# Kernel optimization log

Measured on AMD Instinct MI355X. Metric: run time of the kernel, lower is better.

Reference implementation:

```python
import jax, jax.numpy as jnp
import numpy as np

N_NODES = 50000
N_EDGES = 250000
N_GRAPHS = 512
F_IN = 32
F_EDGE = 16
LATENT = 32
EMBED = 128


def setup_inputs() -> dict:
    key = jax.random.key(0)
    ks = jax.random.split(key, 10)
    x = jax.random.normal(ks[0], (N_NODES, F_IN), dtype=jnp.float32)
    edge_index = jax.random.randint(ks[1], (2, N_EDGES), 0, N_NODES, dtype=jnp.int64)
    edge_attr = jax.random.normal(ks[2], (N_EDGES, F_EDGE), dtype=jnp.float32)
    batch = jnp.sort(jax.random.randint(ks[3], (N_NODES,), 0, N_GRAPHS, dtype=jnp.int64))
    s = 0.05
    W1 = jax.random.normal(ks[4], (F_EDGE, LATENT), dtype=jnp.float32) * s
    b1 = jnp.zeros((LATENT,), jnp.float32)
    W2 = jax.random.normal(ks[5], (LATENT, F_IN * LATENT), dtype=jnp.float32) * s
    b2 = jnp.zeros((F_IN * LATENT,), jnp.float32)
    root = jax.random.normal(ks[6], (F_IN, LATENT), dtype=jnp.float32) * s
    conv_bias = jnp.zeros((LATENT,), jnp.float32)
    fc_w = jax.random.normal(ks[7], (LATENT, EMBED), dtype=jnp.float32) * s
    fc_b = jnp.zeros((EMBED,), jnp.float32)
    return dict(x=x, edge_index=edge_index, edge_attr=edge_attr, batch=batch,
                W1=W1, b1=b1, W2=W2, b2=b2, root=root, conv_bias=conv_bias,
                fc_w=fc_w, fc_b=fc_b)


def reference(x, edge_index, edge_attr, batch, W1, b1, W2, b2, root, conv_bias, fc_w, fc_b):
    src, dst = edge_index[0], edge_index[1]
    # edge MLP: [E, F_edge] -> [E, F_in*latent] -> [E, F_in, latent]
    h = jax.nn.relu(edge_attr @ W1 + b1)
    ew = (h @ W2 + b2).reshape(-1, F_IN, LATENT)
    # per-edge matvec: message_e = x[src_e] @ W_e
    msg = jnp.einsum('ef,efl->el', x[src], ew)
    # scatter-add to target nodes (NNConv default aggr='add')
    agg = jax.ops.segment_sum(msg, dst, num_segments=N_NODES)
    node = jax.nn.relu(agg + x @ root + conv_bias)
    # global mean pool per graph
    sums = jax.ops.segment_sum(node, batch, num_segments=N_GRAPHS)
    cnts = jax.ops.segment_sum(jnp.ones((node.shape[0],), node.dtype), batch, num_segments=N_GRAPHS)
    pooled = sums / jnp.maximum(cnts, 1.0)[:, None]
    return jax.nn.relu(pooled) @ fc_w + fc_b
```

## Files before the change

### kernel.cpp

```cpp
#include <hip/hip_runtime.h>

#define N_NODES 50000
#define N_EDGES 250000
#define N_GRAPHS 512
#define F_IN 32
#define F_EDGE 16
#define LATENT 32
#define EMBED 128
#define E_BLK 128
#define N_EBLK ((N_EDGES + E_BLK - 1) / E_BLK)
#define KW 1056
#define HS_STRIDE 36

typedef unsigned short ushort;
typedef unsigned int uint;
typedef _Float16 half8v __attribute__((ext_vector_type(8)));
typedef _Float16 half2v __attribute__((ext_vector_type(2)));
typedef __attribute__((ext_vector_type(4))) float f32x4;

union UH8 { half8v h8; half2v h2[4]; ushort u[8]; uint q[4]; };
union UH2 { half2v h2; uint q; };

__device__ inline ushort f2h_bits(float f) {
    _Float16 h = (_Float16)f;
    return *reinterpret_cast<ushort*>(&h);
}

__global__ void prep_kernel(const float* __restrict__ x, const float* __restrict__ W2,
                            const float* __restrict__ b2, ushort* __restrict__ xh,
                            ushort* __restrict__ W2T, float4* __restrict__ agg4,
                            float* __restrict__ pool, float* __restrict__ pcnt) {
    int i = blockIdx.x * blockDim.x + threadIdx.x;
    if (i < (N_NODES * F_IN) / 4) {
        float4 v = ((const float4*)x)[i];
        union { ushort u[4]; uint2 q; } pk;
        pk.u[0] = f2h_bits(v.x); pk.u[1] = f2h_bits(v.y);
        pk.u[2] = f2h_bits(v.z); pk.u[3] = f2h_bits(v.w);
        ((uint2*)xh)[i] = pk.q;
    }
    if (i < (N_NODES * LATENT) / 4) agg4[i] = make_float4(0.f, 0.f, 0.f, 0.f);
    if (i < 32 * 1024) {
        int kk = i >> 5, l = i & 31;
        W2T[l * KW + kk] = f2h_bits(W2[i]);
    }
    if (i < 1024) {
        int f = i >> 5, l = i & 31;
        W2T[l * KW + 1024 + f] = f2h_bits(b2[i]);
    }
    if (i < N_GRAPHS * LATENT) pool[i] = 0.f;
    if (i < N_GRAPHS) pcnt[i] = 0.f;
}

__global__ __launch_bounds__(256) void edge_mfma_kernel(
    const ushort* __restrict__ xh, const int* __restrict__ ei,
    const float* __restrict__ ea, const float* __restrict__ W1,
    const float* __restrict__ b1, const ushort* __restrict__ W2T,
    float* __restrict__ agg)
{
    __shared__ __attribute__((aligned(16))) uint Hs2[E_BLK * HS_STRIDE];
    __shared__ __attribute__((aligned(16))) ushort W2q[32 * 256];

    const int t = threadIdx.x;
    const int e0 = blockIdx.x * E_BLK;
    const int wv = t >> 6, lane = t & 63;
    const int g = lane >> 4, j16 = lane & 15;

    UH8 bw[2];
    #pragma unroll
    for (int nt = 0; nt < 2; ++nt) {
        #pragma unroll
        for (int b = 0; b < 8; ++b) {
            float w = (g < 2) ? W1[(8 * g + b) * LATENT + nt * 16 + j16] : 0.f;
            bw[nt].u[b] = f2h_bits(w);
        }
    }
    float b1v[2] = { b1[j16], b1[16 + j16] };

    #pragma unroll
    for (int mt = 0; mt < 2; ++mt) {
        int mtg = 2 * wv + mt;
        int rowA = mtg * 16 + j16;
        int e = e0 + rowA; if (e >= N_EDGES) e = N_EDGES - 1;
        UH8 ae;
        if (g < 2) {
            const float4* p = (const float4*)(ea + (size_t)e * F_EDGE + 8 * g);
            float4 va = p[0], vb = p[1];
            ae.u[0] = f2h_bits(va.x); ae.u[1] = f2h_bits(va.y);
            ae.u[2] = f2h_bits(va.z); ae.u[3] = f2h_bits(va.w);
            ae.u[4] = f2h_bits(vb.x); ae.u[5] = f2h_bits(vb.y);
            ae.u[6] = f2h_bits(vb.z); ae.u[7] = f2h_bits(vb.w);
        } else {
            ae.q[0] = 0; ae.q[1] = 0; ae.q[2] = 0; ae.q[3] = 0;
        }
        #pragma unroll
        for (int nt = 0; nt < 2; ++nt) {
            f32x4 hacc = (f32x4){0.f, 0.f, 0.f, 0.f};
            hacc = __builtin_amdgcn_mfma_f32_16x16x32_f16(ae.h8, bw[nt].h8, hacc, 0, 0, 0);
            #pragma unroll
            for (int v = 0; v < 4; ++v) {
                int rowD = mtg * 16 + 4 * g + v;
                int col = nt * 16 + j16;
                float hval = fmaxf(hacc[v] + b1v[nt], 0.f);
                uint hb = (uint)f2h_bits(hval);
                Hs2[rowD * HS_STRIDE + col] = hb * 0x10001u;
            }
        }
    }
    if (t < E_BLK) Hs2[t * HS_STRIDE + 32] = 0x3C003C00u;

    f32x4 acc[2][2];
    #pragma unroll
    for (int a = 0; a < 2; ++a)
        #pragma unroll
        for (int b = 0; b < 2; ++b) acc[a][b] = (f32x4){0.f, 0.f, 0.f, 0.f};

    UH8 xf[2];
    int myrow[2];
    #pragma unroll
    for (int mt = 0; mt < 2; ++mt) {
        int row = (2 * wv + mt) * 16 + j16;
        myrow[mt] = row;
        int e = e0 + row; if (e >= N_EDGES) e = N_EDGES - 1;
        int src = ei[e];
        uint4 raw = *(const uint4*)(xh + (size_t)src * F_IN + 8 * g);
        xf[mt].q[0] = raw.x; xf[mt].q[1] = raw.y; xf[mt].q[2] = raw.z; xf[mt].q[3] = raw.w;
    }

    {
        UH8 bx0, bx1;
        *(uint4*)bx0.q = *(const uint4*)(W2T + (size_t)j16 * KW + 1024 + 8 * g);
        *(uint4*)bx1.q = *(const uint4*)(W2T + (size_t)(16 + j16) * KW + 1024 + 8 * g);
        #pragma unroll
        for (int mt = 0; mt < 2; ++mt) {
            acc[mt][0] = __builtin_amdgcn_mfma_f32_16x16x32_f16(xf[mt].h8, bx0.h8, acc[mt][0], 0, 0, 0);
            acc[mt][1] = __builtin_amdgcn_mfma_f32_16x16x32_f16(xf[mt].h8, bx1.h8, acc[mt][1], 0, 0, 0);
        }
    }

    __syncthreads();

    for (int q = 0; q < 4; ++q) {
        if (q) __syncthreads();
        #pragma unroll
        for (int c = 0; c < 4; ++c) {
            int ch = c * 256 + t;
            int lbyte = ch * 16;
            int jrow = lbyte >> 9;
            int off = lbyte & 511;
            uint4 val = *(const uint4*)((const char*)W2T + (size_t)jrow * (KW * 2) + q * 512 + off);
            *(uint4*)((char*)W2q + jrow * 512 + (off ^ ((jrow & 7) << 4))) = val;
        }
        __syncthreads();

        uint hb[2][8];
        #pragma unroll
        for (int mt = 0; mt < 2; ++mt) {
            const uint* hp = Hs2 + myrow[mt] * HS_STRIDE + q * 8;
            uint4 a = *(const uint4*)hp;
            uint4 b = *(const uint4*)(hp + 4);
            hb[mt][0] = a.x; hb[mt][1] = a.y; hb[mt][2] = a.z; hb[mt][3] = a.w;
            hb[mt][4] = b.x; hb[mt][5] = b.y; hb[mt][6] = b.z; hb[mt][7] = b.w;
        }

        #pragma unroll
        for (int kst = 0; kst < 8; ++kst) {
            int kb = kst * 64 + g * 16;
            UH8 bf0, bf1;
            *(uint4*)bf0.q = *(const uint4*)((const char*)W2q + j16 * 512 + (kb ^ ((j16 & 7) << 4)));
            *(uint4*)bf1.q = *(const uint4*)((const char*)W2q + (16 + j16) * 512 + (kb ^ ((j16 & 7) << 4)));
            #pragma unroll
            for (int mt = 0; mt < 2; ++mt) {
                UH2 h2; h2.q = hb[mt][kst];
                UH8 af;
                #pragma unroll
                for (int p = 0; p < 4; ++p) af.h2[p] = h2.h2 * xf[mt].h2[p];
                acc[mt][0] = __builtin_amdgcn_mfma_f32_16x16x32_f16(af.h8, bf0.h8, acc[mt][0], 0, 0, 0);
                acc[mt][1] = __builtin_amdgcn_mfma_f32_16x16x32_f16(af.h8, bf1.h8, acc[mt][1], 0, 0, 0);
            }
        }
    }

    #pragma unroll
    for (int mt = 0; mt < 2; ++mt) {
        int rowb = (2 * wv + mt) * 16 + 4 * g;
        #pragma unroll
        for (int v = 0; v < 4; ++v) {
            int e = e0 + rowb + v;
            if (e < N_EDGES) {
                int dst = ei[N_EDGES + e];
                atomicAdd(&agg[(size_t)dst * LATENT + j16],      acc[mt][0][v]);
                atomicAdd(&agg[(size_t)dst * LATENT + 16 + j16], acc[mt][1][v]);
            }
        }
    }
}

#define VN 8
__global__ __launch_bounds__(256) void nodepool_kernel(
    const float* __restrict__ x, const float* __restrict__ agg,
    const float* __restrict__ root, const float* __restrict__ cbias,
    const int* __restrict__ batch, float* __restrict__ pool,
    float* __restrict__ pcnt)
{
    int t = threadIdx.x;
    int l = t & 31;
    int stripe = t >> 5;
    int v0 = (blockIdx.x * 8 + stripe) * VN;
    float rc[F_IN];
    #pragma unroll
    for (int f = 0; f < F_IN; ++f) rc[f] = root[f * LATENT + l];
    float cbl = cbias[l];

    float sum = 0.f, cnt = 0.f;
    int gcur = -1;
    for (int i = 0; i < VN; ++i) {
        int v = v0 + i;
        if (v >= N_NODES) break;
        int g = batch[v];
        if (g != gcur) {
            if (gcur >= 0) {
                atomicAdd(&pool[gcur * LATENT + l], sum);
                if (l == 0) atomicAdd(&pcnt[gcur], cnt);
            }
            gcur = g; sum = 0.f; cnt = 0.f;
        }
        float xv = x[(size_t)v * F_IN + l];
        float a = agg[(size_t)v * LATENT + l] + cbl;
        #pragma unroll
        for (int f = 0; f < F_IN; ++f) {
            float xfv = __shfl(xv, (t & 32) | f);
            a += xfv * rc[f];
        }
        sum += fmaxf(a, 0.f);
        cnt += 1.f;
    }
    if (gcur >= 0) {
        atomicAdd(&pool[gcur * LATENT + l], sum);
        if (l == 0) atomicAdd(&pcnt[gcur], cnt);
    }
}

__global__ void final_kernel(const float* __restrict__ pool, const float* __restrict__ pcnt,
                             const float* __restrict__ fcw, const float* __restrict__ fcb,
                             float* __restrict__ out)
{
    int t = blockIdx.x * blockDim.x + threadIdx.x;
    int gr = t >> 7, j = t & 127;
    if (gr >= N_GRAPHS) return;
    float inv = 1.0f / fmaxf(pcnt[gr], 1.0f);
    float o = fcb[j];
    #pragma unroll 8
    for (int l = 0; l < LATENT; ++l) {
        float pv = fmaxf(pool[gr * LATENT + l] * inv, 0.0f);
        o += pv * fcw[l * EMBED + j];
    }
    out[gr * EMBED + j] = o;
}

extern "C" void kernel_launch(void* const* d_in, const int* in_sizes, int n_in,
                              void* d_out, int out_size, void* d_ws, size_t ws_size,
                              hipStream_t stream)
{
    const float* x     = (const float*)d_in[0];
    const int*   ei    = (const int*)d_in[1];
    const float* ea    = (const float*)d_in[2];
    const int*   batch = (const int*)d_in[3];
    const float* W1    = (const float*)d_in[4];
    const float* b1    = (const float*)d_in[5];
    const float* W2    = (const float*)d_in[6];
    const float* b2    = (const float*)d_in[7];
    const float* root  = (const float*)d_in[8];
    const float* cb    = (const float*)d_in[9];
    const float* fcw   = (const float*)d_in[10];
    const float* fcb   = (const float*)d_in[11];
    float* out = (float*)d_out;

    char* w = (char*)d_ws;
    auto alloc = [&](size_t bytes) {
        char* p = w;
        w += (bytes + 255) & ~size_t(255);
        return p;
    };
    ushort* W2T  = (ushort*)alloc((size_t)32 * KW * 2);
    ushort* xh   = (ushort*)alloc((size_t)N_NODES * F_IN * 2);
    float*  agg  = (float*)alloc((size_t)N_NODES * LATENT * 4);
    float*  pool = (float*)alloc(N_GRAPHS * LATENT * 4);
    float*  pcnt = (float*)alloc(N_GRAPHS * 4);

    prep_kernel<<<1563, 256, 0, stream>>>(x, W2, b2, xh, W2T, (float4*)agg, pool, pcnt);
    edge_mfma_kernel<<<N_EBLK, 256, 0, stream>>>(xh, ei, ea, W1, b1, W2T, agg);
    nodepool_kernel<<<(N_NODES + 8 * VN - 1) / (8 * VN), 256, 0, stream>>>(
        x, agg, root, cb, batch, pool, pcnt);
    final_kernel<<<(N_GRAPHS * EMBED + 255) / 256, 256, 0, stream>>>(pool, pcnt, fcw, fcb, out);
}
```

Measured before the change: 77.57 us.

## Bucket edges by destination tile and fuse node update with edge kernel

Builds a CSR-like bucketing of edges by destination-node tile (64 nodes) with histogram, scan and scatter kernels. The edge kernel then processes each tile's edges, accumulates messages in shared-memory atomics, and performs the root transform, ReLU and pooling in the same block. This removes the global agg buffer, its zeroing and the global float atomics. In exchange it adds three small kernels (one single-block scan), indirect gathers through csr, partially filled 128-edge chunks, and uneven per-tile work.

New measurement: 249.0 us. 221% more time.

```diff
diff --git a/kernel.cpp b/kernel.cpp
--- a/kernel.cpp
+++ b/kernel.cpp
@@ -7,10 +7,12 @@
 #define F_EDGE 16
 #define LATENT 32
 #define EMBED 128
-#define E_BLK 128
-#define N_EBLK ((N_EDGES + E_BLK - 1) / E_BLK)
+#define DT 64
+#define NB ((N_NODES + DT - 1) / DT)
+#define EC 128
 #define KW 1056
 #define HS_STRIDE 36
+#define AGG_S 33
 
 typedef unsigned short ushort;
 typedef unsigned int uint;
@@ -28,7 +30,7 @@
 
 __global__ void prep_kernel(const float* __restrict__ x, const float* __restrict__ W2,
                             const float* __restrict__ b2, ushort* __restrict__ xh,
-                            ushort* __restrict__ W2T, float4* __restrict__ agg4,
+                            ushort* __restrict__ W2T, int* __restrict__ deg,
                             float* __restrict__ pool, float* __restrict__ pcnt) {
     int i = blockIdx.x * blockDim.x + threadIdx.x;
     if (i < (N_NODES * F_IN) / 4) {
@@ -38,7 +40,6 @@
         pk.u[2] = f2h_bits(v.z); pk.u[3] = f2h_bits(v.w);
         ((uint2*)xh)[i] = pk.q;
     }
-    if (i < (N_NODES * LATENT) / 4) agg4[i] = make_float4(0.f, 0.f, 0.f, 0.f);
     if (i < 32 * 1024) {
         int kk = i >> 5, l = i & 31;
         W2T[l * KW + kk] = f2h_bits(W2[i]);
@@ -47,23 +48,77 @@
         int f = i >> 5, l = i & 31;
         W2T[l * KW + 1024 + f] = f2h_bits(b2[i]);
     }
+    if (i < NB) deg[i] = 0;
     if (i < N_GRAPHS * LATENT) pool[i] = 0.f;
     if (i < N_GRAPHS) pcnt[i] = 0.f;
+}
+
+__global__ void hist_kernel(const int* __restrict__ ei, int* __restrict__ deg) {
+    int e = blockIdx.x * blockDim.x + threadIdx.x;
+    if (e < N_EDGES) atomicAdd(&deg[ei[N_EDGES + e] / DT], 1);
+}
+
+__global__ __launch_bounds__(1024) void scan_kernel(const int* __restrict__ deg,
+                                                    int* __restrict__ off,
+                                                    int* __restrict__ cursor) {
+    __shared__ int wsum[16];
+    int t = threadIdx.x;
+    int d = (t < NB) ? deg[t] : 0;
+    int lane = t & 63, wid = t >> 6;
+    int inc = d;
+    #pragma unroll
+    for (int s = 1; s < 64; s <<= 1) {
+        int o = __shfl_up(inc, s);
+        if (lane >= s) inc += o;
+    }
+    if (lane == 63) wsum[wid] = inc;
+    __syncthreads();
+    if (t < 16) {
+        int w = wsum[t];
+        int winc = w;
+        #pragma unroll
+        for (int s = 1; s < 16; s <<= 1) {
+            int o = __shfl_up(winc, s);
+            if (t >= s) winc += o;
+        }
+        wsum[t] = winc - w;
+    }
+    __syncthreads();
+    int base = wsum[wid] + (inc - d);
+    if (t < NB) { off[t] = base; cursor[t] = base; }
+    if (t == 1023) off[NB] = base + d;
+}
+
+__global__ void scatter_kernel(const int* __restrict__ ei, int* __restrict__ cursor,
+                               int* __restrict__ csr) {
+    int e = blockIdx.x * blockDim.x + threadIdx.x;
+    if (e < N_EDGES) {
+        int p = atomicAdd(&cursor[ei[N_EDGES + e] / DT], 1);
+        csr[p] = e;
+    }
 }
 
 __global__ __launch_bounds__(256) void edge_mfma_kernel(
     const ushort* __restrict__ xh, const int* __restrict__ ei,
     const float* __restrict__ ea, const float* __restrict__ W1,
     const float* __restrict__ b1, const ushort* __restrict__ W2T,
-    float* __restrict__ agg)
+    const int* __restrict__ off, const int* __restrict__ csr,
+    const float* __restrict__ x, const float* __restrict__ root,
+    const float* __restrict__ cbias, const int* __restrict__ batch,
+    float* __restrict__ pool, float* __restrict__ pcnt)
 {
-    __shared__ __attribute__((aligned(16))) uint Hs2[E_BLK * HS_STRIDE];
+    __shared__ __attribute__((aligned(16))) uint Hs2[EC * HS_STRIDE];
     __shared__ __attribute__((aligned(16))) ushort W2q[32 * 256];
+    __shared__ float aggL[DT * AGG_S];
 
     const int t = threadIdx.x;
-    const int e0 = blockIdx.x * E_BLK;
+    const int v0 = blockIdx.x * DT;
     const int wv = t >> 6, lane = t & 63;
     const int g = lane >> 4, j16 = lane & 15;
+    const int estart = off[blockIdx.x];
+    const int eend = off[blockIdx.x + 1];
+
+    for (int i = t; i < DT * AGG_S; i += 256) aggL[i] = 0.f;
 
     UH8 bw[2];
     #pragma unroll
@@ -75,168 +130,168 @@
         }
     }
     float b1v[2] = { b1[j16], b1[16 + j16] };
-
-    #pragma unroll
-    for (int mt = 0; mt < 2; ++mt) {
-        int mtg = 2 * wv + mt;
-        int rowA = mtg * 16 + j16;
-        int e = e0 + rowA; if (e >= N_EDGES) e = N_EDGES - 1;
-        UH8 ae;
-        if (g < 2) {
-            const float4* p = (const float4*)(ea + (size_t)e * F_EDGE + 8 * g);
-            float4 va = p[0], vb = p[1];
-            ae.u[0] = f2h_bits(va.x); ae.u[1] = f2h_bits(va.y);
-            ae.u[2] = f2h_bits(va.z); ae.u[3] = f2h_bits(va.w);
-            ae.u[4] = f2h_bits(vb.x); ae.u[5] = f2h_bits(vb.y);
-            ae.u[6] = f2h_bits(vb.z); ae.u[7] = f2h_bits(vb.w);
-        } else {
-            ae.q[0] = 0; ae.q[1] = 0; ae.q[2] = 0; ae.q[3] = 0;
-        }
-        #pragma unroll
-        for (int nt = 0; nt < 2; ++nt) {
-            f32x4 hacc = (f32x4){0.f, 0.f, 0.f, 0.f};
-            hacc = __builtin_amdgcn_mfma_f32_16x16x32_f16(ae.h8, bw[nt].h8, hacc, 0, 0, 0);
-            #pragma unroll
-            for (int v = 0; v < 4; ++v) {
-                int rowD = mtg * 16 + 4 * g + v;
-                int col = nt * 16 + j16;
-                float hval = fmaxf(hacc[v] + b1v[nt], 0.f);
-                uint hb = (uint)f2h_bits(hval);
-                Hs2[rowD * HS_STRIDE + col] = hb * 0x10001u;
-            }
-        }
-    }
-    if (t < E_BLK) Hs2[t * HS_STRIDE + 32] = 0x3C003C00u;
-
-    f32x4 acc[2][2];
-    #pragma unroll
-    for (int a = 0; a < 2; ++a)
-        #pragma unroll
-        for (int b = 0; b < 2; ++b) acc[a][b] = (f32x4){0.f, 0.f, 0.f, 0.f};
-
-    UH8 xf[2];
-    int myrow[2];
-    #pragma unroll
-    for (int mt = 0; mt < 2; ++mt) {
-        int row = (2 * wv + mt) * 16 + j16;
-        myrow[mt] = row;
-        int e = e0 + row; if (e >= N_EDGES) e = N_EDGES - 1;
-        int src = ei[e];
-        uint4 raw = *(const uint4*)(xh + (size_t)src * F_IN + 8 * g);
-        xf[mt].q[0] = raw.x; xf[mt].q[1] = raw.y; xf[mt].q[2] = raw.z; xf[mt].q[3] = raw.w;
-    }
-
-    {
-        UH8 bx0, bx1;
-        *(uint4*)bx0.q = *(const uint4*)(W2T + (size_t)j16 * KW + 1024 + 8 * g);
-        *(uint4*)bx1.q = *(const uint4*)(W2T + (size_t)(16 + j16) * KW + 1024 + 8 * g);
+    UH8 bx0, bx1;
+    *(uint4*)bx0.q = *(const uint4*)(W2T + (size_t)j16 * KW + 1024 + 8 * g);
+    *(uint4*)bx1.q = *(const uint4*)(W2T + (size_t)(16 + j16) * KW + 1024 + 8 * g);
+
+    __syncthreads();
+
+    for (int cs = estart; cs < eend; cs += EC) {
+        int nE = eend - cs; if (nE > EC) nE = EC;
+
+        #pragma unroll
+        for (int mt = 0; mt < 2; ++mt) {
+            int mtg = 2 * wv + mt;
+            int rowA = mtg * 16 + j16;
+            int p = cs + rowA; if (p >= eend) p = eend - 1;
+            int e = csr[p];
+            UH8 ae;
+            if (g < 2) {
+                const float4* pp = (const float4*)(ea + (size_t)e * F_EDGE + 8 * g);
+                float4 va = pp[0], vb = pp[1];
+                ae.u[0] = f2h_bits(va.x); ae.u[1] = f2h_bits(va.y);
+                ae.u[2] = f2h_bits(va.z); ae.u[3] = f2h_bits(va.w);
+                ae.u[4] = f2h_bits(vb.x); ae.u[5] = f2h_bits(vb.y);
+                ae.u[6] = f2h_bits(vb.z); ae.u[7] = f2h_bits(vb.w);
+            } else {
+                ae.q[0] = 0; ae.q[1] = 0; ae.q[2] = 0; ae.q[3] = 0;
+            }
+            #pragma unroll
+            for (int nt = 0; nt < 2; ++nt) {
+                f32x4 hacc = (f32x4){0.f, 0.f, 0.f, 0.f};
+                hacc = __builtin_amdgcn_mfma_f32_16x16x32_f16(ae.h8, bw[nt].h8, hacc, 0, 0, 0);
+                #pragma unroll
+                for (int v = 0; v < 4; ++v) {
+                    int rowD = mtg * 16 + 4 * g + v;
+                    int col = nt * 16 + j16;
+                    float hval = fmaxf(hacc[v] + b1v[nt], 0.f);
+                    uint hb = (uint)f2h_bits(hval);
+                    Hs2[rowD * HS_STRIDE + col] = hb * 0x10001u;
+                }
+            }
+        }
+        if (t < EC) Hs2[t * HS_STRIDE + 32] = 0x3C003C00u;
+
+        f32x4 acc[2][2];
+        #pragma unroll
+        for (int a = 0; a < 2; ++a)
+            #pragma unroll
+            for (int b = 0; b < 2; ++b) acc[a][b] = (f32x4){0.f, 0.f, 0.f, 0.f};
+
+        UH8 xf[2];
+        int myrow[2];
+        #pragma unroll
+        for (int mt = 0; mt < 2; ++mt) {
+            int row = (2 * wv + mt) * 16 + j16;
+            myrow[mt] = row;
+            int p = cs + row; if (p >= eend) p = eend - 1;
+            int src = ei[csr[p]];
+            uint4 raw = *(const uint4*)(xh + (size_t)src * F_IN + 8 * g);
+            xf[mt].q[0] = raw.x; xf[mt].q[1] = raw.y; xf[mt].q[2] = raw.z; xf[mt].q[3] = raw.w;
+        }
+
         #pragma unroll
         for (int mt = 0; mt < 2; ++mt) {
             acc[mt][0] = __builtin_amdgcn_mfma_f32_16x16x32_f16(xf[mt].h8, bx0.h8, acc[mt][0], 0, 0, 0);
             acc[mt][1] = __builtin_amdgcn_mfma_f32_16x16x32_f16(xf[mt].h8, bx1.h8, acc[mt][1], 0, 0, 0);
         }
-    }
-
-    __syncthreads();
-
-    for (int q = 0; q < 4; ++q) {
-        if (q) __syncthreads();
-        #pragma unroll
-        for (int c = 0; c < 4; ++c) {
-            int ch = c * 256 + t;
-            int lbyte = ch * 16;
-            int jrow = lbyte >> 9;
-            int off = lbyte & 511;
-            uint4 val = *(const uint4*)((const char*)W2T + (size_t)jrow * (KW * 2) + q * 512 + off);
-            *(uint4*)((char*)W2q + jrow * 512 + (off ^ ((jrow & 7) << 4))) = val;
-        }
+
         __syncthreads();
 
-        uint hb[2][8];
+        for (int q = 0; q < 4; ++q) {
+            if (q) __syncthreads();
+            #pragma unroll
+            for (int c = 0; c < 4; ++c) {
+                int ch = c * 256 + t;
+                int lbyte = ch * 16;
+                int jrow = lbyte >> 9;
+                int offb = lbyte & 511;
+                uint4 val = *(const uint4*)((const char*)W2T + (size_t)jrow * (KW * 2) + q * 512 + offb);
+                *(uint4*)((char*)W2q + jrow * 512 + (offb ^ ((jrow & 7) << 4))) = val;
+            }
+            __syncthreads();
+
+            uint hb[2][8];
+            #pragma unroll
+            for (int mt = 0; mt < 2; ++mt) {
+                const uint* hp = Hs2 + myrow[mt] * HS_STRIDE + q * 8;
+                uint4 a = *(const uint4*)hp;
+                uint4 b = *(const uint4*)(hp + 4);
+                hb[mt][0] = a.x; hb[mt][1] = a.y; hb[mt][2] = a.z; hb[mt][3] = a.w;
+                hb[mt][4] = b.x; hb[mt][5] = b.y; hb[mt][6] = b.z; hb[mt][7] = b.w;
+            }
+
+            #pragma unroll
+            for (int kst = 0; kst < 8; ++kst) {
+                int kb = kst * 64 + g * 16;
+                UH8 bf0, bf1;
+                *(uint4*)bf0.q = *(const uint4*)((const char*)W2q + j16 * 512 + (kb ^ ((j16 & 7) << 4)));
+                *(uint4*)bf1.q = *(const uint4*)((const char*)W2q + (16 + j16) * 512 + (kb ^ ((j16 & 7) << 4)));
+                #pragma unroll
+                for (int mt = 0; mt < 2; ++mt) {
+                    UH2 h2; h2.q = hb[mt][kst];
+                    UH8 af;
+                    #pragma unroll
+                    for (int p = 0; p < 4; ++p) af.h2[p] = h2.h2 * xf[mt].h2[p];
+                    acc[mt][0] = __builtin_amdgcn_mfma_f32_16x16x32_f16(af.h8, bf0.h8, acc[mt][0], 0, 0, 0);
+                    acc[mt][1] = __builtin_amdgcn_mfma_f32_16x16x32_f16(af.h8, bf1.h8, acc[mt][1], 0, 0, 0);
+                }
+            }
+        }
+
         #pragma unroll
         for (int mt = 0; mt < 2; ++mt) {
-            const uint* hp = Hs2 + myrow[mt] * HS_STRIDE + q * 8;
-            uint4 a = *(const uint4*)hp;
-            uint4 b = *(const uint4*)(hp + 4);
-            hb[mt][0] = a.x; hb[mt][1] = a.y; hb[mt][2] = a.z; hb[mt][3] = a.w;
-            hb[mt][4] = b.x; hb[mt][5] = b.y; hb[mt][6] = b.z; hb[mt][7] = b.w;
-        }
-
-        #pragma unroll
-        for (int kst = 0; kst < 8; ++kst) {
-            int kb = kst * 64 + g * 16;
-            UH8 bf0, bf1;
-            *(uint4*)bf0.q = *(const uint4*)((const char*)W2q + j16 * 512 + (kb ^ ((j16 & 7) << 4)));
-            *(uint4*)bf1.q = *(const uint4*)((const char*)W2q + (16 + j16) * 512 + (kb ^ ((j16 & 7) << 4)));
-            #pragma unroll
-            for (int mt = 0; mt < 2; ++mt) {
-                UH2 h2; h2.q = hb[mt][kst];
-                UH8 af;
-                #pragma unroll
-                for (int p = 0; p < 4; ++p) af.h2[p] = h2.h2 * xf[mt].h2[p];
-                acc[mt][0] = __builtin_amdgcn_mfma_f32_16x16x32_f16(af.h8, bf0.h8, acc[mt][0], 0, 0, 0);
-                acc[mt][1] = __builtin_amdgcn_mfma_f32_16x16x32_f16(af.h8, bf1.h8, acc[mt][1], 0, 0, 0);
-            }
-        }
-    }
-
-    #pragma unroll
-    for (int mt = 0; mt < 2; ++mt) {
-        int rowb = (2 * wv + mt) * 16 + 4 * g;
-        #pragma unroll
-        for (int v = 0; v < 4; ++v) {
-            int e = e0 + rowb + v;
-            if (e < N_EDGES) {
-                int dst = ei[N_EDGES + e];
-                atomicAdd(&agg[(size_t)dst * LATENT + j16],      acc[mt][0][v]);
-                atomicAdd(&agg[(size_t)dst * LATENT + 16 + j16], acc[mt][1][v]);
-            }
-        }
-    }
-}
-
-#define VN 8
-__global__ __launch_bounds__(256) void nodepool_kernel(
-    const float* __restrict__ x, const float* __restrict__ agg,
-    const float* __restrict__ root, const float* __restrict__ cbias,
-    const int* __restrict__ batch, float* __restrict__ pool,
-    float* __restrict__ pcnt)
-{
-    int t = threadIdx.x;
-    int l = t & 31;
-    int stripe = t >> 5;
-    int v0 = (blockIdx.x * 8 + stripe) * VN;
-    float rc[F_IN];
-    #pragma unroll
-    for (int f = 0; f < F_IN; ++f) rc[f] = root[f * LATENT + l];
-    float cbl = cbias[l];
-
-    float sum = 0.f, cnt = 0.f;
-    int gcur = -1;
-    for (int i = 0; i < VN; ++i) {
-        int v = v0 + i;
-        if (v >= N_NODES) break;
-        int g = batch[v];
-        if (g != gcur) {
-            if (gcur >= 0) {
-                atomicAdd(&pool[gcur * LATENT + l], sum);
-                if (l == 0) atomicAdd(&pcnt[gcur], cnt);
-            }
-            gcur = g; sum = 0.f; cnt = 0.f;
-        }
-        float xv = x[(size_t)v * F_IN + l];
-        float a = agg[(size_t)v * LATENT + l] + cbl;
-        #pragma unroll
-        for (int f = 0; f < F_IN; ++f) {
-            float xfv = __shfl(xv, (t & 32) | f);
-            a += xfv * rc[f];
-        }
-        sum += fmaxf(a, 0.f);
-        cnt += 1.f;
-    }
-    if (gcur >= 0) {
-        atomicAdd(&pool[gcur * LATENT + l], sum);
-        if (l == 0) atomicAdd(&pcnt[gcur], cnt);
+            int rowb = (2 * wv + mt) * 16 + 4 * g;
+            #pragma unroll
+            for (int v = 0; v < 4; ++v) {
+                int row = rowb + v;
+                if (row < nE) {
+                    int e = csr[cs + row];
+                    int n = ei[N_EDGES + e] - v0;
+                    atomicAdd(&aggL[n * AGG_S + j16],      acc[mt][0][v]);
+                    atomicAdd(&aggL[n * AGG_S + 16 + j16], acc[mt][1][v]);
+                }
+            }
+        }
+        __syncthreads();
+    }
+
+    {
+        int l = t & 31;
+        int stripe = t >> 5;
+        int vb = v0 + stripe * 8;
+        float rc[F_IN];
+        #pragma unroll
+        for (int f = 0; f < F_IN; ++f) rc[f] = root[f * LATENT + l];
+        float cbl = cbias[l];
+
+        float sum = 0.f, cnt = 0.f;
+        int gcur = -1;
+        for (int i = 0; i < 8; ++i) {
+            int v = vb + i;
+            if (v >= N_NODES) break;
+            int gr = batch[v];
+            if (gr != gcur) {
+                if (gcur >= 0) {
+                    atomicAdd(&pool[gcur * LATENT + l], sum);
+                    if (l == 0) atomicAdd(&pcnt[gcur], cnt);
+                }
+                gcur = gr; sum = 0.f; cnt = 0.f;
+            }
+            float xv = x[(size_t)v * F_IN + l];
+            float a = aggL[(v - v0) * AGG_S + l] + cbl;
+            #pragma unroll
+            for (int f = 0; f < F_IN; ++f) {
+                float xfv = __shfl(xv, (t & 32) | f);
+                a += xfv * rc[f];
+            }
+            sum += fmaxf(a, 0.f);
+            cnt += 1.f;
+        }
+        if (gcur >= 0) {
+            atomicAdd(&pool[gcur * LATENT + l], sum);
+            if (l == 0) atomicAdd(&pcnt[gcur], cnt);
+        }
     }
 }
 
@@ -281,15 +336,20 @@
         w += (bytes + 255) & ~size_t(255);
         return p;
     };
-    ushort* W2T  = (ushort*)alloc((size_t)32 * KW * 2);
-    ushort* xh   = (ushort*)alloc((size_t)N_NODES * F_IN * 2);
-    float*  agg  = (float*)alloc((size_t)N_NODES * LATENT * 4);
-    float*  pool = (float*)alloc(N_GRAPHS * LATENT * 4);
-    float*  pcnt = (float*)alloc(N_GRAPHS * 4);
-
-    prep_kernel<<<1563, 256, 0, stream>>>(x, W2, b2, xh, W2T, (float4*)agg, pool, pcnt);
-    edge_mfma_kernel<<<N_EBLK, 256, 0, stream>>>(xh, ei, ea, W1, b1, W2T, agg);
-    nodepool_kernel<<<(N_NODES + 8 * VN - 1) / (8 * VN), 256, 0, stream>>>(
-        x, agg, root, cb, batch, pool, pcnt);
+    ushort* W2T    = (ushort*)alloc((size_t)32 * KW * 2);
+    ushort* xh     = (ushort*)alloc((size_t)N_NODES * F_IN * 2);
+    int*    deg    = (int*)alloc(NB * 4);
+    int*    off    = (int*)alloc((NB + 1) * 4);
+    int*    cursor = (int*)alloc(NB * 4);
+    int*    csr    = (int*)alloc(N_EDGES * 4);
+    float*  pool   = (float*)alloc(N_GRAPHS * LATENT * 4);
+    float*  pcnt   = (float*)alloc(N_GRAPHS * 4);
+
+    prep_kernel<<<1563, 256, 0, stream>>>(x, W2, b2, xh, W2T, deg, pool, pcnt);
+    hist_kernel<<<(N_EDGES + 255) / 256, 256, 0, stream>>>(ei, deg);
+    scan_kernel<<<1, 1024, 0, stream>>>(deg, off, cursor);
+    scatter_kernel<<<(N_EDGES + 255) / 256, 256, 0, stream>>>(ei, cursor, csr);
+    edge_mfma_kernel<<<NB, 256, 0, stream>>>(xh, ei, ea, W1, b1, W2T, off, csr,
+                                             x, root, cb, batch, pool, pcnt);
     final_kernel<<<(N_GRAPHS * EMBED + 255) / 256, 256, 0, stream>>>(pool, pcnt, fcw, fcb, out);
 }
```
